# Kernel tuning notes

Measured on AMD Instinct MI355X. Metric: run time of the kernel, lower is better.

## Reference

```python
import jax, jax.numpy as jnp
import numpy as np

D1, D2, ADD1, ADD2 = 32, 32, 16, 16
BATCH = 8


def _photon_basis(m, p):
    """All occupation tuples of m modes with p photons, first mode counts descending."""
    basis = []
    def gen(modes, rem, prefix):
        if modes == 1:
            basis.append(prefix + (rem,))
            return
        for k in range(rem, -1, -1):
            gen(modes - 1, rem - k, prefix + (k,))
    gen(m, p, ())
    return basis


def _fock_index_map(d1, d2, add1, add2):
    m = d1 + d2 + add1 + add2
    basis = _photon_basis(m, 2)
    index = {s: i for i, s in enumerate(basis)}
    idx = np.empty(d1 * d2, dtype=np.int64)
    for i in range(d1):
        for j in range(d2):
            s = [0] * m
            s[add1 + i] = 1
            s[add1 + d1 + j] = 1
            idx[i * d2 + j] = index[tuple(s)]
    return idx, len(basis)  # len(basis) == m*(m+1)//2


def setup_inputs() -> dict:
    key = jax.random.key(0)
    idx, fock_dim = _fock_index_map(D1, D2, ADD1, ADD2)
    n = D1 * D2  # 1024
    input_state = jax.random.normal(key, (BATCH, n, n), dtype=jnp.float32)
    return {
        "input_state": input_state,
        "fock_idx": jnp.asarray(idx),   # [n] int64, one Fock index per image-basis element
        "fock_dim": fock_dim,           # static int: 4656
    }


def reference(input_state, fock_idx, fock_dim):
    # P @ rho @ P^T where P[:, c] is one-hot at fock_idx[c].
    # Equivalent to scattering rho[b, i, j] into out[b, fock_idx[i], fock_idx[j]].
    B = input_state.shape[0]
    out = jnp.zeros((B, fock_dim, fock_dim), dtype=input_state.dtype)
    return out.at[:, fock_idx[:, None], fock_idx[None, :]].set(input_state)
```

## Files before the change

### kernel.cpp

```cpp
#include <hip/hip_runtime.h>

constexpr int FOCK_DIM = 4656;
constexpr int N        = 1024;
constexpr int ROW_VEC  = FOCK_DIM / 4;

typedef float f32x4 __attribute__((ext_vector_type(4)));
typedef int   i32x4 __attribute__((ext_vector_type(4)));

__global__ __launch_bounds__(256) void init_inv_kernel(int* __restrict__ inv) {
    int i = blockIdx.x * 256 + threadIdx.x;
    if (i < FOCK_DIM) inv[i] = -1;
}

__global__ __launch_bounds__(256) void fill_inv_kernel(const int* __restrict__ fock_idx,
                                                       int* __restrict__ inv) {
    int i = blockIdx.x * 256 + threadIdx.x;
    if (i < N) inv[fock_idx[i]] = i;
}

__global__ __launch_bounds__(256) void scatter_rows_kernel(
    const float* __restrict__ in,
    const int*   __restrict__ inv,
    float*       __restrict__ out) {

    const int br  = blockIdx.x;
    const int b   = br / FOCK_DIM;
    const int r   = br - b * FOCK_DIM;
    const int x   = inv[r];

    f32x4* __restrict__ orow = reinterpret_cast<f32x4*>(out + (size_t)br * FOCK_DIM);

    if (x < 0) {
        const f32x4 z = {0.f, 0.f, 0.f, 0.f};
        for (int c4 = threadIdx.x; c4 < ROW_VEC; c4 += 256) {
            orow[c4] = z;
        }
        return;
    }

    const float* __restrict__ irow = in + ((size_t)b * N + (size_t)x) * N;
    const i32x4* __restrict__ inv4 = reinterpret_cast<const i32x4*>(inv);
    for (int c4 = threadIdx.x; c4 < ROW_VEC; c4 += 256) {
        const i32x4 iv = inv4[c4];
        f32x4 v;
        v.x = (iv.x >= 0) ? irow[iv.x] : 0.f;
        v.y = (iv.y >= 0) ? irow[iv.y] : 0.f;
        v.z = (iv.z >= 0) ? irow[iv.z] : 0.f;
        v.w = (iv.w >= 0) ? irow[iv.w] : 0.f;
        orow[c4] = v;
    }
}

extern "C" void kernel_launch(void* const* d_in, const int* in_sizes, int n_in,
                              void* d_out, int out_size, void* d_ws, size_t ws_size,
                              hipStream_t stream) {
    const float* in       = (const float*)d_in[0];
    const int*   fock_idx = (const int*)d_in[1];
    float*       out      = (float*)d_out;
    int*         inv      = (int*)d_ws;

    const int B = in_sizes[0] / (N * N);

    init_inv_kernel<<<(FOCK_DIM + 255) / 256, 256, 0, stream>>>(inv);
    fill_inv_kernel<<<(N + 255) / 256, 256, 0, stream>>>(fock_idx, inv);
    scatter_rows_kernel<<<B * FOCK_DIM, 256, 0, stream>>>(in, inv, out);
}
```

Measured before the change: 153.4 us.

## Replace per-row scatter blocks with flat grid-stride scatter kernel

The one-block-per-output-row launch (about 37k blocks of 256 threads, most of which loop only partly full over 1164 vectors) is replaced by a fixed 2048-block grid-stride loop over every float4 of the output. Each element recomputes its row and batch with integer divides and looks up inv per element. This aims to cut block scheduling overhead and tail waste in what is a write-bound 694 MB fill. It hardcodes batch 8 instead of deriving it from the input size, and it adds per-element div/mod and inv loads.

```diff
diff --git a/kernel.cpp b/kernel.cpp
--- a/kernel.cpp
+++ b/kernel.cpp
@@ -3,6 +3,10 @@
 constexpr int FOCK_DIM = 4656;
 constexpr int N        = 1024;
 constexpr int ROW_VEC  = FOCK_DIM / 4;
+constexpr int B        = 8;
+constexpr unsigned TOTAL4 = (unsigned)B * FOCK_DIM * (unsigned)ROW_VEC;
+constexpr int GRID  = 2048;
+constexpr int BLOCK = 256;
 
 typedef float f32x4 __attribute__((ext_vector_type(4)));
 typedef int   i32x4 __attribute__((ext_vector_type(4)));
@@ -18,36 +22,32 @@
     if (i < N) inv[fock_idx[i]] = i;
 }
 
-__global__ __launch_bounds__(256) void scatter_rows_kernel(
+__global__ __launch_bounds__(BLOCK) void flat_scatter_kernel(
     const float* __restrict__ in,
     const int*   __restrict__ inv,
     float*       __restrict__ out) {
 
-    const int br  = blockIdx.x;
-    const int b   = br / FOCK_DIM;
-    const int r   = br - b * FOCK_DIM;
-    const int x   = inv[r];
+    const i32x4* __restrict__ inv4 = reinterpret_cast<const i32x4*>(inv);
+    f32x4*       __restrict__ out4 = reinterpret_cast<f32x4*>(out);
 
-    f32x4* __restrict__ orow = reinterpret_cast<f32x4*>(out + (size_t)br * FOCK_DIM);
+    #pragma unroll 2
+    for (unsigned f = blockIdx.x * BLOCK + threadIdx.x; f < TOTAL4; f += GRID * BLOCK) {
+        const unsigned row = f / ROW_VEC;
+        const unsigned c4  = f - row * ROW_VEC;
+        const unsigned b   = row / FOCK_DIM;
+        const unsigned r   = row - b * FOCK_DIM;
+        const int x = inv[r];
 
-    if (x < 0) {
-        const f32x4 z = {0.f, 0.f, 0.f, 0.f};
-        for (int c4 = threadIdx.x; c4 < ROW_VEC; c4 += 256) {
-            orow[c4] = z;
+        f32x4 v = {0.f, 0.f, 0.f, 0.f};
+        if (x >= 0) {
+            const i32x4 iv = inv4[c4];
+            const float* __restrict__ irow = in + ((size_t)b * N + (size_t)x) * N;
+            v.x = (iv.x >= 0) ? irow[iv.x] : 0.f;
+            v.y = (iv.y >= 0) ? irow[iv.y] : 0.f;
+            v.z = (iv.z >= 0) ? irow[iv.z] : 0.f;
+            v.w = (iv.w >= 0) ? irow[iv.w] : 0.f;
         }
-        return;
-    }
-
-    const float* __restrict__ irow = in + ((size_t)b * N + (size_t)x) * N;
-    const i32x4* __restrict__ inv4 = reinterpret_cast<const i32x4*>(inv);
-    for (int c4 = threadIdx.x; c4 < ROW_VEC; c4 += 256) {
-        const i32x4 iv = inv4[c4];
-        f32x4 v;
-        v.x = (iv.x >= 0) ? irow[iv.x] : 0.f;
-        v.y = (iv.y >= 0) ? irow[iv.y] : 0.f;
-        v.z = (iv.z >= 0) ? irow[iv.z] : 0.f;
-        v.w = (iv.w >= 0) ? irow[iv.w] : 0.f;
-        orow[c4] = v;
+        out4[f] = v;
     }
 }
 
@@ -59,9 +59,7 @@
     float*       out      = (float*)d_out;
     int*         inv      = (int*)d_ws;
 
-    const int B = in_sizes[0] / (N * N);
-
     init_inv_kernel<<<(FOCK_DIM + 255) / 256, 256, 0, stream>>>(inv);
     fill_inv_kernel<<<(N + 255) / 256, 256, 0, stream>>>(fock_idx, inv);
-    scatter_rows_kernel<<<B * FOCK_DIM, 256, 0, stream>>>(in, inv, out);
+    flat_scatter_kernel<<<GRID, BLOCK, 0, stream>>>(in, inv, out);
 }
```

Result: slower. 177.7 us (+15.8%).

## Scatter live rows through LDS with coalesced input reads, separate dead-row zero blocks

Applied to the files above, without the earlier changes.

Live output rows are now produced by blocks indexed by input row. Each block reads its input row with coalesced vector loads, scatters it into a zeroed LDS row using fock_idx, and writes the full row out. Dead rows are zero-filled by a second range of blocks in the same launch, which return early for live rows. This replaces the per-element gathered global reads of the old kernel, but it hardcodes the batch size and adds extra blocks that exit immediately.

```diff
diff --git a/kernel.cpp b/kernel.cpp
--- a/kernel.cpp
+++ b/kernel.cpp
@@ -3,6 +3,9 @@
 constexpr int FOCK_DIM = 4656;
 constexpr int N        = 1024;
 constexpr int ROW_VEC  = FOCK_DIM / 4;
+constexpr int B        = 8;
+constexpr int NBLK_LIVE = B * N;
+constexpr int NBLK_DEAD = B * FOCK_DIM;
 
 typedef float f32x4 __attribute__((ext_vector_type(4)));
 typedef int   i32x4 __attribute__((ext_vector_type(4)));
@@ -18,37 +21,52 @@
     if (i < N) inv[fock_idx[i]] = i;
 }
 
-__global__ __launch_bounds__(256) void scatter_rows_kernel(
+__global__ __launch_bounds__(256) void scatter_main_kernel(
     const float* __restrict__ in,
+    const int*   __restrict__ fock_idx,
     const int*   __restrict__ inv,
     float*       __restrict__ out) {
 
-    const int br  = blockIdx.x;
-    const int b   = br / FOCK_DIM;
-    const int r   = br - b * FOCK_DIM;
-    const int x   = inv[r];
+    const int tid = threadIdx.x;
+    int blk = blockIdx.x;
 
-    f32x4* __restrict__ orow = reinterpret_cast<f32x4*>(out + (size_t)br * FOCK_DIM);
+    if (blk < NBLK_LIVE) {
+        const int b = blk >> 10;
+        const int i = blk & (N - 1);
 
-    if (x < 0) {
+        const f32x4 vin = reinterpret_cast<const f32x4*>(
+            in + ((size_t)b * N + (size_t)i) * N)[tid];
+        const i32x4 fc = reinterpret_cast<const i32x4*>(fock_idx)[tid];
+        const int r = fock_idx[i];
+
+        __shared__ float ldsrow[FOCK_DIM];
+        f32x4* lds4 = reinterpret_cast<f32x4*>(ldsrow);
         const f32x4 z = {0.f, 0.f, 0.f, 0.f};
-        for (int c4 = threadIdx.x; c4 < ROW_VEC; c4 += 256) {
-            orow[c4] = z;
-        }
+        #pragma unroll
+        for (int c4 = tid; c4 < ROW_VEC; c4 += 256) lds4[c4] = z;
+        __syncthreads();
+
+        ldsrow[fc.x] = vin.x;
+        ldsrow[fc.y] = vin.y;
+        ldsrow[fc.z] = vin.z;
+        ldsrow[fc.w] = vin.w;
+        __syncthreads();
+
+        f32x4* orow = reinterpret_cast<f32x4*>(
+            out + ((size_t)b * FOCK_DIM + (size_t)r) * FOCK_DIM);
+        for (int c4 = tid; c4 < ROW_VEC; c4 += 256) orow[c4] = lds4[c4];
         return;
     }
 
-    const float* __restrict__ irow = in + ((size_t)b * N + (size_t)x) * N;
-    const i32x4* __restrict__ inv4 = reinterpret_cast<const i32x4*>(inv);
-    for (int c4 = threadIdx.x; c4 < ROW_VEC; c4 += 256) {
-        const i32x4 iv = inv4[c4];
-        f32x4 v;
-        v.x = (iv.x >= 0) ? irow[iv.x] : 0.f;
-        v.y = (iv.y >= 0) ? irow[iv.y] : 0.f;
-        v.z = (iv.z >= 0) ? irow[iv.z] : 0.f;
-        v.w = (iv.w >= 0) ? irow[iv.w] : 0.f;
-        orow[c4] = v;
-    }
+    blk -= NBLK_LIVE;
+    const int b = blk / FOCK_DIM;
+    const int r = blk - b * FOCK_DIM;
+    if (inv[r] >= 0) return;
+
+    f32x4* orow = reinterpret_cast<f32x4*>(
+        out + ((size_t)b * FOCK_DIM + (size_t)r) * FOCK_DIM);
+    const f32x4 z = {0.f, 0.f, 0.f, 0.f};
+    for (int c4 = tid; c4 < ROW_VEC; c4 += 256) orow[c4] = z;
 }
 
 extern "C" void kernel_launch(void* const* d_in, const int* in_sizes, int n_in,
@@ -59,9 +77,7 @@
     float*       out      = (float*)d_out;
     int*         inv      = (int*)d_ws;
 
-    const int B = in_sizes[0] / (N * N);
-
     init_inv_kernel<<<(FOCK_DIM + 255) / 256, 256, 0, stream>>>(inv);
     fill_inv_kernel<<<(N + 255) / 256, 256, 0, stream>>>(fock_idx, inv);
-    scatter_rows_kernel<<<B * FOCK_DIM, 256, 0, stream>>>(in, inv, out);
+    scatter_main_kernel<<<NBLK_LIVE + NBLK_DEAD, 256, 0, stream>>>(in, fock_idx, inv, out);
 }
```

After: 152.9 us. About the same (-0.3%).

## Fuse inverse-map build into persistent scatter kernel with LDS inverse table

Applied to the files above, without the earlier changes.

The separate init and fill kernels are removed. Each persistent block now builds the inverse Fock index map in shared memory and then loops over output rows with a fixed 2048-block grid. This drops two extra launches and the global-memory inverse lookups, in exchange for every block rebuilding the table redundantly. Batch size is now a hardcoded constant, and fock_idx is read as int32 with exactly 256 threads covering 1024 entries.

```diff
diff --git a/kernel.cpp b/kernel.cpp
--- a/kernel.cpp
+++ b/kernel.cpp
@@ -3,51 +3,58 @@
 constexpr int FOCK_DIM = 4656;
 constexpr int N        = 1024;
 constexpr int ROW_VEC  = FOCK_DIM / 4;
+constexpr int B        = 8;
+constexpr int TOTROWS  = B * FOCK_DIM;
+constexpr int GRID     = 2048;
+constexpr int BLOCK    = 256;
 
 typedef float f32x4 __attribute__((ext_vector_type(4)));
 typedef int   i32x4 __attribute__((ext_vector_type(4)));
 
-__global__ __launch_bounds__(256) void init_inv_kernel(int* __restrict__ inv) {
-    int i = blockIdx.x * 256 + threadIdx.x;
-    if (i < FOCK_DIM) inv[i] = -1;
-}
-
-__global__ __launch_bounds__(256) void fill_inv_kernel(const int* __restrict__ fock_idx,
-                                                       int* __restrict__ inv) {
-    int i = blockIdx.x * 256 + threadIdx.x;
-    if (i < N) inv[fock_idx[i]] = i;
-}
-
-__global__ __launch_bounds__(256) void scatter_rows_kernel(
+__global__ __launch_bounds__(BLOCK, 8) void fock_scatter_kernel(
     const float* __restrict__ in,
-    const int*   __restrict__ inv,
+    const int*   __restrict__ fock_idx,
     float*       __restrict__ out) {
 
-    const int br  = blockIdx.x;
-    const int b   = br / FOCK_DIM;
-    const int r   = br - b * FOCK_DIM;
-    const int x   = inv[r];
+    __shared__ __align__(16) int inv_lds[FOCK_DIM];
+    const int tid = threadIdx.x;
 
-    f32x4* __restrict__ orow = reinterpret_cast<f32x4*>(out + (size_t)br * FOCK_DIM);
-
-    if (x < 0) {
-        const f32x4 z = {0.f, 0.f, 0.f, 0.f};
-        for (int c4 = threadIdx.x; c4 < ROW_VEC; c4 += 256) {
-            orow[c4] = z;
-        }
-        return;
+    i32x4* inv4_lds = reinterpret_cast<i32x4*>(inv_lds);
+    {
+        const i32x4 mone = {-1, -1, -1, -1};
+        for (int t = tid; t < ROW_VEC; t += BLOCK) inv4_lds[t] = mone;
+        __syncthreads();
+        const i32x4 fc = reinterpret_cast<const i32x4*>(fock_idx)[tid];
+        inv_lds[fc.x] = 4 * tid + 0;
+        inv_lds[fc.y] = 4 * tid + 1;
+        inv_lds[fc.z] = 4 * tid + 2;
+        inv_lds[fc.w] = 4 * tid + 3;
+        __syncthreads();
     }
 
-    const float* __restrict__ irow = in + ((size_t)b * N + (size_t)x) * N;
-    const i32x4* __restrict__ inv4 = reinterpret_cast<const i32x4*>(inv);
-    for (int c4 = threadIdx.x; c4 < ROW_VEC; c4 += 256) {
-        const i32x4 iv = inv4[c4];
-        f32x4 v;
-        v.x = (iv.x >= 0) ? irow[iv.x] : 0.f;
-        v.y = (iv.y >= 0) ? irow[iv.y] : 0.f;
-        v.z = (iv.z >= 0) ? irow[iv.z] : 0.f;
-        v.w = (iv.w >= 0) ? irow[iv.w] : 0.f;
-        orow[c4] = v;
+    for (int br = blockIdx.x; br < TOTROWS; br += GRID) {
+        const int b = br / FOCK_DIM;
+        const int r = br - b * FOCK_DIM;
+        const int x = inv_lds[r];
+
+        f32x4* __restrict__ orow =
+            reinterpret_cast<f32x4*>(out + (size_t)br * FOCK_DIM);
+
+        if (x < 0) {
+            const f32x4 z = {0.f, 0.f, 0.f, 0.f};
+            for (int c4 = tid; c4 < ROW_VEC; c4 += BLOCK) orow[c4] = z;
+        } else {
+            const float* __restrict__ irow = in + ((size_t)b * N + (size_t)x) * N;
+            for (int c4 = tid; c4 < ROW_VEC; c4 += BLOCK) {
+                const i32x4 iv = inv4_lds[c4];
+                f32x4 v;
+                v.x = (iv.x >= 0) ? irow[iv.x] : 0.f;
+                v.y = (iv.y >= 0) ? irow[iv.y] : 0.f;
+                v.z = (iv.z >= 0) ? irow[iv.z] : 0.f;
+                v.w = (iv.w >= 0) ? irow[iv.w] : 0.f;
+                orow[c4] = v;
+            }
+        }
     }
 }
 
@@ -57,11 +64,6 @@
     const float* in       = (const float*)d_in[0];
     const int*   fock_idx = (const int*)d_in[1];
     float*       out      = (float*)d_out;
-    int*         inv      = (int*)d_ws;
 
-    const int B = in_sizes[0] / (N * N);
-
-    init_inv_kernel<<<(FOCK_DIM + 255) / 256, 256, 0, stream>>>(inv);
-    fill_inv_kernel<<<(N + 255) / 256, 256, 0, stream>>>(fock_idx, inv);
-    scatter_rows_kernel<<<B * FOCK_DIM, 256, 0, stream>>>(in, inv, out);
+    fock_scatter_kernel<<<GRID, BLOCK, 0, stream>>>(in, fock_idx, out);
 }
```

Result: slower. 175.4 us (+14.3%).
